# Kernel tuning notes

Hardware: AMD Instinct MI355X
Metric: run time of the kernel (lower is better)

The kernel has to match this reference:

```python
import jax, jax.numpy as jnp
import numpy as np

N, D_IN, D_OUT = 4096, 1024, 1024


def setup_inputs() -> dict:
    key = jax.random.key(0)
    kx, kq, kk, kv = jax.random.split(key, 4)
    s = 1.0 / np.sqrt(D_IN)
    return {
        "x": jax.random.normal(kx, (N, D_IN), dtype=jnp.float32),
        "Wq": jax.random.normal(kq, (D_OUT, D_IN), dtype=jnp.float32) * s,
        "Wk": jax.random.normal(kk, (D_OUT, D_IN), dtype=jnp.float32) * s,
        "Wv": jax.random.normal(kv, (D_OUT, D_IN), dtype=jnp.float32) * s,
    }


def reference(x, Wq, Wk, Wv):
    # nn.Linear(d_in, d_out, bias=False): y = x @ W.T with W: [d_out, d_in]
    q = x @ Wq.T            # [N, d_out]
    k = x @ Wk.T            # [N, d_out]
    v = x @ Wv.T            # [N, d_out]
    scores = q @ k.T        # [N, N]
    scale = 1.0 / jnp.sqrt(jnp.asarray(k.shape[-1], dtype=x.dtype))
    attn = jax.nn.softmax(scores * scale, axis=-1)
    return attn @ v         # [N, d_out]
```

## Files before the change

### kernel.cpp

```cpp
#include <hip/hip_runtime.h>


typedef __attribute__((ext_vector_type(8))) __bf16 bf16x8;
typedef __attribute__((ext_vector_type(4))) float floatx4;

#define GLB_AS __attribute__((address_space(1)))
#define LDS_AS __attribute__((address_space(3)))

static __device__ __forceinline__ unsigned short f2bf_u16(float f) {
  union { float f; unsigned u; } x; x.f = f;
  unsigned r = x.u;
  r += 0x7fffu + ((r >> 16) & 1u);
  return (unsigned short)(r >> 16);
}
static __device__ __forceinline__ float bf2f(unsigned short u) {
  union { unsigned u; float f; } x; x.u = ((unsigned)u) << 16; return x.f;
}

__global__ __launch_bounds__(256) void zero_rs(float* __restrict__ rs) {
  ((float4*)rs)[blockIdx.x * 256 + threadIdx.x] = make_float4(0.f, 0.f, 0.f, 0.f);
}

__global__ __launch_bounds__(256) void cast_all(const float* __restrict__ x,
                                                const float* __restrict__ Wq,
                                                const float* __restrict__ Wk,
                                                const float* __restrict__ Wv,
                                                unsigned short* __restrict__ xb,
                                                unsigned short* __restrict__ wb) {
  const int i = blockIdx.x * 256 + threadIdx.x;
  const int NX4 = 4096 * 1024 / 4;
  const int NW4 = 1024 * 1024 / 4;
  const float* src; unsigned short* dst; int k;
  if (i < NX4)                { src = x;  dst = xb; k = i; }
  else if (i < NX4 + NW4)     { src = Wq; dst = wb;                 k = i - NX4; }
  else if (i < NX4 + 2 * NW4) { src = Wk; dst = wb + 1024 * 1024;   k = i - NX4 - NW4; }
  else                        { src = Wv; dst = wb + 2 * 1024 * 1024; k = i - NX4 - 2 * NW4; }
  float4 v = reinterpret_cast<const float4*>(src)[k];
  ushort4 o = make_ushort4(f2bf_u16(v.x), f2bf_u16(v.y), f2bf_u16(v.z), f2bf_u16(v.w));
  reinterpret_cast<ushort4*>(dst)[k] = o;
}

struct GemmOuts { void* c[4]; int ldc[4]; };

template <int EPI>
__global__ __launch_bounds__(512, 2) void gemm256(const unsigned short* __restrict__ A,
                                                  const unsigned short* __restrict__ B,
                                                  GemmOuts outs, int lda, int ldb,
                                                  int klen, float scale) {
  __shared__ unsigned short sh[65536];
  const int t = threadIdx.x;
  const int w = t >> 6, lane = t & 63;
  const int wm = w >> 2, wn = w & 3;
  const int gx = gridDim.x;
  const int nwg = gx * gridDim.y;
  int bid = blockIdx.y * gx + blockIdx.x;
  bid = (bid & 7) * (nwg >> 3) + (bid >> 3);
  const int row0 = (bid / gx) * 256;
  const int col0 = (bid % gx) * 256;
  const int z = blockIdx.z;
  const int kstart = z * klen;
  const int NT = klen >> 6;

  const int scbe = (((t & 3) ^ ((t >> 3) & 3)) << 3);
  const unsigned short* gA0 = A + (size_t)(row0 + (t >> 2)) * lda + kstart + scbe;
  const unsigned short* gA1 = gA0 + (size_t)128 * lda;
  const unsigned short* gB0 = B + (size_t)(col0 + (t >> 2)) * ldb + kstart + scbe;
  const unsigned short* gB1 = gB0 + (size_t)128 * ldb;

#define STAGE_HALF(h_) do { \
    const int tile_ = (h_) >> 2, opb_ = (h_) & 1, kh_ = ((h_) >> 1) & 1; \
    const int lo_ = (((tile_) & 1) << 15) + (opb_ << 14) + (kh_ << 13) + (w << 9); \
    const unsigned short* s0_ = (opb_ ? gB0 : gA0) + tile_ * 64 + kh_ * 32; \
    const unsigned short* s1_ = (opb_ ? gB1 : gA1) + tile_ * 64 + kh_ * 32; \
    __builtin_amdgcn_global_load_lds((const GLB_AS void*)s0_, (LDS_AS void*)&sh[lo_], 16, 0, 0); \
    __builtin_amdgcn_global_load_lds((const GLB_AS void*)s1_, (LDS_AS void*)&sh[lo_ + 4096], 16, 0, 0); \
  } while (0)
#define STAGE_IF(h_) do { const int hh_ = (h_); if (hh_ < 4 * NT) STAGE_HALF(hh_); } while (0)

  const int fr = lane & 15;
  const int sg = (((lane >> 4) ^ ((lane >> 1) & 3)) << 3);
  int aofs[8], bofs[4];
#pragma unroll
  for (int mf = 0; mf < 8; ++mf) aofs[mf] = ((wm * 128 + mf * 16 + fr) << 5) + sg;
#pragma unroll
  for (int nf = 0; nf < 4; ++nf) bofs[nf] = 16384 + ((wn * 64 + nf * 16 + fr) << 5) + sg;

  floatx4 acc[8][4] = {};

#pragma unroll
  for (int h = 0; h < 7; ++h) STAGE_IF(h);
  asm volatile("s_waitcnt vmcnt(6)" ::: "memory");
  __builtin_amdgcn_s_barrier();

  for (int tile = 0; tile < NT; ++tile) {
    const int bo = (tile & 1) << 15;
    bf16x8 a0[8], b0[2], b1[2];

#pragma unroll
    for (int mf = 0; mf < 8; ++mf) a0[mf] = *(const bf16x8*)&sh[bo + aofs[mf]];
    b0[0] = *(const bf16x8*)&sh[bo + bofs[0]];
    b0[1] = *(const bf16x8*)&sh[bo + bofs[1]];
    STAGE_IF(4 * tile + 7);
    __builtin_amdgcn_s_barrier();
    asm volatile("s_waitcnt lgkmcnt(0)" ::: "memory");
    __builtin_amdgcn_sched_barrier(0);
    __builtin_amdgcn_s_setprio(1);
#pragma unroll
    for (int mf = 0; mf < 8; ++mf)
#pragma unroll
      for (int nf = 0; nf < 2; ++nf)
        acc[mf][nf] = __builtin_amdgcn_mfma_f32_16x16x32_bf16(a0[mf], b0[nf], acc[mf][nf], 0, 0, 0);
    __builtin_amdgcn_s_setprio(0);
    __builtin_amdgcn_s_barrier();

    b1[0] = *(const bf16x8*)&sh[bo + bofs[2]];
    b1[1] = *(const bf16x8*)&sh[bo + bofs[3]];
    STAGE_IF(4 * tile + 8);
    __builtin_amdgcn_s_barrier();
    asm volatile("s_waitcnt lgkmcnt(0)" ::: "memory");
    __builtin_amdgcn_sched_barrier(0);
    __builtin_amdgcn_s_setprio(1);
#pragma unroll
    for (int mf = 0; mf < 8; ++mf)
#pragma unroll
      for (int nf = 0; nf < 2; ++nf)
        acc[mf][2 + nf] = __builtin_amdgcn_mfma_f32_16x16x32_bf16(a0[mf], b1[nf], acc[mf][2 + nf], 0, 0, 0);
    __builtin_amdgcn_s_setprio(0);
    __builtin_amdgcn_s_barrier();

#pragma unroll
    for (int mf = 0; mf < 8; ++mf) a0[mf] = *(const bf16x8*)&sh[bo + 8192 + aofs[mf]];
    b0[0] = *(const bf16x8*)&sh[bo + 8192 + bofs[0]];
    b0[1] = *(const bf16x8*)&sh[bo + 8192 + bofs[1]];
    STAGE_IF(4 * tile + 9);
    __builtin_amdgcn_s_barrier();
    asm volatile("s_waitcnt lgkmcnt(0)" ::: "memory");
    __builtin_amdgcn_sched_barrier(0);
    __builtin_amdgcn_s_setprio(1);
#pragma unroll
    for (int mf = 0; mf < 8; ++mf)
#pragma unroll
      for (int nf = 0; nf < 2; ++nf)
        acc[mf][nf] = __builtin_amdgcn_mfma_f32_16x16x32_bf16(a0[mf], b0[nf], acc[mf][nf], 0, 0, 0);
    __builtin_amdgcn_s_setprio(0);
    __builtin_amdgcn_s_barrier();

    b1[0] = *(const bf16x8*)&sh[bo + 8192 + bofs[2]];
    b1[1] = *(const bf16x8*)&sh[bo + 8192 + bofs[3]];
    STAGE_IF(4 * tile + 10);
    __builtin_amdgcn_s_barrier();
    asm volatile("s_waitcnt lgkmcnt(0)" ::: "memory");
    __builtin_amdgcn_sched_barrier(0);
    __builtin_amdgcn_s_setprio(1);
#pragma unroll
    for (int mf = 0; mf < 8; ++mf)
#pragma unroll
      for (int nf = 0; nf < 2; ++nf)
        acc[mf][2 + nf] = __builtin_amdgcn_mfma_f32_16x16x32_bf16(a0[mf], b1[nf], acc[mf][2 + nf], 0, 0, 0);
    __builtin_amdgcn_s_setprio(0);
    if (tile < NT - 2)       { asm volatile("s_waitcnt vmcnt(6)" ::: "memory"); }
    else if (tile == NT - 2) { asm volatile("s_waitcnt vmcnt(0)" ::: "memory"); }
    __builtin_amdgcn_s_barrier();
  }

#undef STAGE_HALF
#undef STAGE_IF

  const int er = (lane >> 4) * 4;
  const int ec = lane & 15;

  if (EPI == 0) {
    if (z == 0) {
      float* Cf = (float*)outs.c[0];
      const int ldc = outs.ldc[0];
#pragma unroll
      for (int mf = 0; mf < 8; ++mf)
#pragma unroll
        for (int nf = 0; nf < 4; ++nf)
#pragma unroll
          for (int r = 0; r < 4; ++r)
            Cf[(size_t)(row0 + wm * 128 + mf * 16 + er + r) * ldc +
               (col0 + wn * 64 + nf * 16 + ec)] = acc[mf][nf][r] * scale;
    } else {
      unsigned short* Cb = (unsigned short*)outs.c[z];
      const int ldc = outs.ldc[z];
#pragma unroll
      for (int mf = 0; mf < 8; ++mf)
#pragma unroll
        for (int nf = 0; nf < 4; ++nf)
#pragma unroll
          for (int r = 0; r < 4; ++r)
            Cb[(size_t)(row0 + wm * 128 + mf * 16 + er + r) * ldc +
               (col0 + wn * 64 + nf * 16 + ec)] = f2bf_u16(acc[mf][nf][r] * scale);
    }
  } else if (EPI == 2) {
    unsigned short* Pb = (unsigned short*)outs.c[0];
    float* rsp = (float*)outs.c[1];
    const int ldc = outs.ldc[0];
#pragma unroll
    for (int mf = 0; mf < 8; ++mf) {
#pragma unroll
      for (int r = 0; r < 4; ++r) {
        const int m = row0 + wm * 128 + mf * 16 + er + r;
        float rsum = 0.f;
#pragma unroll
        for (int nf = 0; nf < 4; ++nf) {
          const float e = __expf(acc[mf][nf][r] * scale);
          Pb[(size_t)m * ldc + (col0 + wn * 64 + nf * 16 + ec)] = f2bf_u16(e);
          rsum += e;
        }
        rsum += __shfl_xor(rsum, 1);
        rsum += __shfl_xor(rsum, 2);
        rsum += __shfl_xor(rsum, 4);
        rsum += __shfl_xor(rsum, 8);
        if (ec == 0) atomicAdd(rsp + m, rsum);
      }
    }
  } else {
    if (col0 < 2048) {
      unsigned short* qkb = (unsigned short*)outs.c[0];
#pragma unroll
      for (int mf = 0; mf < 8; ++mf)
#pragma unroll
        for (int nf = 0; nf < 4; ++nf)
#pragma unroll
          for (int r = 0; r < 4; ++r)
            qkb[(size_t)(row0 + wm * 128 + mf * 16 + er + r) * 2048 +
                (col0 + wn * 64 + nf * 16 + ec)] = f2bf_u16(acc[mf][nf][r] * scale);
    } else {
      unsigned short* vT = (unsigned short*)outs.c[1];
#pragma unroll
      for (int mf = 0; mf < 8; ++mf)
#pragma unroll
        for (int nf = 0; nf < 4; ++nf) {
          const int n = (col0 - 2048) + wn * 64 + nf * 16 + ec;
          const int mb = row0 + wm * 128 + mf * 16 + er;
          ushort4 o = make_ushort4(f2bf_u16(acc[mf][nf][0] * scale),
                                   f2bf_u16(acc[mf][nf][1] * scale),
                                   f2bf_u16(acc[mf][nf][2] * scale),
                                   f2bf_u16(acc[mf][nf][3] * scale));
          *reinterpret_cast<ushort4*>(&vT[(size_t)n * 4096 + mb]) = o;
        }
    }
  }
}

__global__ __launch_bounds__(256) void reduce_pv(float* __restrict__ out,
                                                 const unsigned short* __restrict__ p1,
                                                 const unsigned short* __restrict__ p2,
                                                 const unsigned short* __restrict__ p3,
                                                 const float* __restrict__ rs) {
  const int row = blockIdx.x;
  const int idx = row * 256 + threadIdx.x;
  const float inv = 1.0f / rs[row];
  float4 o = ((const float4*)out)[idx];
  ushort4 a = ((const ushort4*)p1)[idx];
  ushort4 b = ((const ushort4*)p2)[idx];
  ushort4 c = ((const ushort4*)p3)[idx];
  o.x = (o.x + bf2f(a.x) + bf2f(b.x) + bf2f(c.x)) * inv;
  o.y = (o.y + bf2f(a.y) + bf2f(b.y) + bf2f(c.y)) * inv;
  o.z = (o.z + bf2f(a.z) + bf2f(b.z) + bf2f(c.z)) * inv;
  o.w = (o.w + bf2f(a.w) + bf2f(b.w) + bf2f(c.w)) * inv;
  ((float4*)out)[idx] = o;
}

extern "C" void kernel_launch(void* const* d_in, const int* in_sizes, int n_in,
                              void* d_out, int out_size, void* d_ws, size_t ws_size,
                              hipStream_t stream) {
  const float* x  = (const float*)d_in[0];
  const float* Wq = (const float*)d_in[1];
  const float* Wk = (const float*)d_in[2];
  const float* Wv = (const float*)d_in[3];
  float* out = (float*)d_out;

  const int N = 4096, D = 1024;

  char* ws = (char*)d_ws;
  unsigned short* P   = (unsigned short*)ws;
  unsigned short* qkb = (unsigned short*)(ws + (32u << 20));
  unsigned short* vT  = (unsigned short*)(ws + (48u << 20));
  unsigned short* xb  = (unsigned short*)(ws + (56u << 20));
  unsigned short* wb  = (unsigned short*)(ws + (64u << 20));
  float*          rs  = (float*)(ws + (70u << 20));
  unsigned short* p1  = (unsigned short*)(ws + (72u << 20));
  unsigned short* p2  = (unsigned short*)(ws + (80u << 20));
  unsigned short* p3  = (unsigned short*)(ws + (88u << 20));

  zero_rs<<<4, 256, 0, stream>>>(rs);

  cast_all<<<7168, 256, 0, stream>>>(x, Wq, Wk, Wv, xb, wb);

  GemmOuts oq; oq.c[0] = qkb; oq.c[1] = vT; oq.c[2] = oq.c[3] = qkb;
  oq.ldc[0] = 2048; oq.ldc[1] = 4096; oq.ldc[2] = oq.ldc[3] = 2048;
  gemm256<3><<<dim3(3 * D / 256, N / 256, 1), 512, 0, stream>>>(xb, wb, oq, D, D, D, 1.0f);

  GemmOuts os; os.c[0] = P; os.c[1] = rs; os.c[2] = os.c[3] = P;
  os.ldc[0] = N; os.ldc[1] = 0; os.ldc[2] = os.ldc[3] = N;
  gemm256<2><<<dim3(N / 256, N / 256, 1), 512, 0, stream>>>(qkb, qkb + D, os, 2 * D, 2 * D, D, 0.03125f);

  GemmOuts op;
  op.c[0] = out; op.ldc[0] = D;
  op.c[1] = p1;  op.ldc[1] = D;
  op.c[2] = p2;  op.ldc[2] = D;
  op.c[3] = p3;  op.ldc[3] = D;
  gemm256<0><<<dim3(D / 256, N / 256, 4), 512, 0, stream>>>(P, vT, op, N, N, N / 4, 1.0f);

  reduce_pv<<<N, 256, 0, stream>>>(out, p1, p2, p3, rs);
}
```

Measured before the change: 150.4 us.

## Shrink GEMM tiles to 128x128 and replace atomic row-sum with partial buffer

Replaces the 256x256, 512-thread GEMM with a 128x128, 256-thread kernel that uses a simple double-buffered K=32 pipeline and a smaller LDS footprint, so more blocks fit per CU. Softmax row sums are written as per-column-block partials and reduced in reduce_pv, which removes the zero_rs launch and the atomics. All four split-K PV partials are now bf16, with the first reusing the xb buffer. The smaller tiles add global and LDS traffic per FLOP and drop the fine-grained setprio/sched_barrier interleaving, and storing the first partial in bf16 lowers precision.

```diff
diff --git a/kernel.cpp b/kernel.cpp
--- a/kernel.cpp
+++ b/kernel.cpp
@@ -15,10 +15,6 @@
 }
 static __device__ __forceinline__ float bf2f(unsigned short u) {
   union { unsigned u; float f; } x; x.u = ((unsigned)u) << 16; return x.f;
-}
-
-__global__ __launch_bounds__(256) void zero_rs(float* __restrict__ rs) {
-  ((float4*)rs)[blockIdx.x * 256 + threadIdx.x] = make_float4(0.f, 0.f, 0.f, 0.f);
 }
 
 __global__ __launch_bounds__(256) void cast_all(const float* __restrict__ x,
@@ -31,9 +27,9 @@
   const int NX4 = 4096 * 1024 / 4;
   const int NW4 = 1024 * 1024 / 4;
   const float* src; unsigned short* dst; int k;
-  if (i < NX4)                { src = x;  dst = xb; k = i; }
-  else if (i < NX4 + NW4)     { src = Wq; dst = wb;                 k = i - NX4; }
-  else if (i < NX4 + 2 * NW4) { src = Wk; dst = wb + 1024 * 1024;   k = i - NX4 - NW4; }
+  if (i < NX4)                { src = x;  dst = xb;                   k = i; }
+  else if (i < NX4 + NW4)     { src = Wq; dst = wb;                   k = i - NX4; }
+  else if (i < NX4 + 2 * NW4) { src = Wk; dst = wb + 1024 * 1024;     k = i - NX4 - NW4; }
   else                        { src = Wv; dst = wb + 2 * 1024 * 1024; k = i - NX4 - 2 * NW4; }
   float4 v = reinterpret_cast<const float4*>(src)[k];
   ushort4 o = make_ushort4(f2bf_u16(v.x), f2bf_u16(v.y), f2bf_u16(v.z), f2bf_u16(v.w));
@@ -43,165 +39,104 @@
 struct GemmOuts { void* c[4]; int ldc[4]; };
 
 template <int EPI>
-__global__ __launch_bounds__(512, 2) void gemm256(const unsigned short* __restrict__ A,
+__global__ __launch_bounds__(256, 4) void gemm128(const unsigned short* __restrict__ A,
                                                   const unsigned short* __restrict__ B,
                                                   GemmOuts outs, int lda, int ldb,
                                                   int klen, float scale) {
-  __shared__ unsigned short sh[65536];
+  __shared__ unsigned short sh[16384];
   const int t = threadIdx.x;
   const int w = t >> 6, lane = t & 63;
-  const int wm = w >> 2, wn = w & 3;
+  const int wm = w >> 1, wn = w & 1;
   const int gx = gridDim.x;
   const int nwg = gx * gridDim.y;
   int bid = blockIdx.y * gx + blockIdx.x;
   bid = (bid & 7) * (nwg >> 3) + (bid >> 3);
-  const int row0 = (bid / gx) * 256;
-  const int col0 = (bid % gx) * 256;
+  const int row0 = (bid / gx) * 128;
+  const int col0 = (bid % gx) * 128;
   const int z = blockIdx.z;
   const int kstart = z * klen;
-  const int NT = klen >> 6;
-
+  const int NT = klen >> 5;
+
+  const int srow = t >> 2;
   const int scbe = (((t & 3) ^ ((t >> 3) & 3)) << 3);
-  const unsigned short* gA0 = A + (size_t)(row0 + (t >> 2)) * lda + kstart + scbe;
-  const unsigned short* gA1 = gA0 + (size_t)128 * lda;
-  const unsigned short* gB0 = B + (size_t)(col0 + (t >> 2)) * ldb + kstart + scbe;
-  const unsigned short* gB1 = gB0 + (size_t)128 * ldb;
-
-#define STAGE_HALF(h_) do { \
-    const int tile_ = (h_) >> 2, opb_ = (h_) & 1, kh_ = ((h_) >> 1) & 1; \
-    const int lo_ = (((tile_) & 1) << 15) + (opb_ << 14) + (kh_ << 13) + (w << 9); \
-    const unsigned short* s0_ = (opb_ ? gB0 : gA0) + tile_ * 64 + kh_ * 32; \
-    const unsigned short* s1_ = (opb_ ? gB1 : gA1) + tile_ * 64 + kh_ * 32; \
-    __builtin_amdgcn_global_load_lds((const GLB_AS void*)s0_, (LDS_AS void*)&sh[lo_], 16, 0, 0); \
-    __builtin_amdgcn_global_load_lds((const GLB_AS void*)s1_, (LDS_AS void*)&sh[lo_ + 4096], 16, 0, 0); \
+  const unsigned short* gA0 = A + (size_t)(row0 + srow) * lda + kstart + scbe;
+  const unsigned short* gA1 = gA0 + (size_t)64 * lda;
+  const unsigned short* gB0 = B + (size_t)(col0 + srow) * ldb + kstart + scbe;
+  const unsigned short* gB1 = gB0 + (size_t)64 * ldb;
+
+#define STAGE(tl_) do { \
+    const int bb_ = ((tl_) & 1) * 8192; \
+    __builtin_amdgcn_global_load_lds((const GLB_AS void*)(gA0 + (tl_) * 32), \
+        (LDS_AS void*)&sh[bb_ + t * 8], 16, 0, 0); \
+    __builtin_amdgcn_global_load_lds((const GLB_AS void*)(gA1 + (tl_) * 32), \
+        (LDS_AS void*)&sh[bb_ + 2048 + t * 8], 16, 0, 0); \
+    __builtin_amdgcn_global_load_lds((const GLB_AS void*)(gB0 + (tl_) * 32), \
+        (LDS_AS void*)&sh[bb_ + 4096 + t * 8], 16, 0, 0); \
+    __builtin_amdgcn_global_load_lds((const GLB_AS void*)(gB1 + (tl_) * 32), \
+        (LDS_AS void*)&sh[bb_ + 6144 + t * 8], 16, 0, 0); \
   } while (0)
-#define STAGE_IF(h_) do { const int hh_ = (h_); if (hh_ < 4 * NT) STAGE_HALF(hh_); } while (0)
 
   const int fr = lane & 15;
   const int sg = (((lane >> 4) ^ ((lane >> 1) & 3)) << 3);
-  int aofs[8], bofs[4];
-#pragma unroll
-  for (int mf = 0; mf < 8; ++mf) aofs[mf] = ((wm * 128 + mf * 16 + fr) << 5) + sg;
-#pragma unroll
-  for (int nf = 0; nf < 4; ++nf) bofs[nf] = 16384 + ((wn * 64 + nf * 16 + fr) << 5) + sg;
-
-  floatx4 acc[8][4] = {};
-
-#pragma unroll
-  for (int h = 0; h < 7; ++h) STAGE_IF(h);
-  asm volatile("s_waitcnt vmcnt(6)" ::: "memory");
-  __builtin_amdgcn_s_barrier();
+  int aofs[4], bofs[4];
+#pragma unroll
+  for (int mf = 0; mf < 4; ++mf) aofs[mf] = ((wm * 64 + mf * 16 + fr) << 5) + sg;
+#pragma unroll
+  for (int nf = 0; nf < 4; ++nf) bofs[nf] = 4096 + ((wn * 64 + nf * 16 + fr) << 5) + sg;
+
+  floatx4 acc[4][4] = {};
+
+  STAGE(0);
 
   for (int tile = 0; tile < NT; ++tile) {
-    const int bo = (tile & 1) << 15;
-    bf16x8 a0[8], b0[2], b1[2];
-
-#pragma unroll
-    for (int mf = 0; mf < 8; ++mf) a0[mf] = *(const bf16x8*)&sh[bo + aofs[mf]];
-    b0[0] = *(const bf16x8*)&sh[bo + bofs[0]];
-    b0[1] = *(const bf16x8*)&sh[bo + bofs[1]];
-    STAGE_IF(4 * tile + 7);
+    if (tile + 1 < NT) {
+      STAGE(tile + 1);
+      asm volatile("s_waitcnt vmcnt(4)" ::: "memory");
+    } else {
+      asm volatile("s_waitcnt vmcnt(0)" ::: "memory");
+    }
     __builtin_amdgcn_s_barrier();
-    asm volatile("s_waitcnt lgkmcnt(0)" ::: "memory");
-    __builtin_amdgcn_sched_barrier(0);
-    __builtin_amdgcn_s_setprio(1);
-#pragma unroll
-    for (int mf = 0; mf < 8; ++mf)
-#pragma unroll
-      for (int nf = 0; nf < 2; ++nf)
-        acc[mf][nf] = __builtin_amdgcn_mfma_f32_16x16x32_bf16(a0[mf], b0[nf], acc[mf][nf], 0, 0, 0);
-    __builtin_amdgcn_s_setprio(0);
-    __builtin_amdgcn_s_barrier();
-
-    b1[0] = *(const bf16x8*)&sh[bo + bofs[2]];
-    b1[1] = *(const bf16x8*)&sh[bo + bofs[3]];
-    STAGE_IF(4 * tile + 8);
-    __builtin_amdgcn_s_barrier();
-    asm volatile("s_waitcnt lgkmcnt(0)" ::: "memory");
-    __builtin_amdgcn_sched_barrier(0);
-    __builtin_amdgcn_s_setprio(1);
-#pragma unroll
-    for (int mf = 0; mf < 8; ++mf)
-#pragma unroll
-      for (int nf = 0; nf < 2; ++nf)
-        acc[mf][2 + nf] = __builtin_amdgcn_mfma_f32_16x16x32_bf16(a0[mf], b1[nf], acc[mf][2 + nf], 0, 0, 0);
-    __builtin_amdgcn_s_setprio(0);
-    __builtin_amdgcn_s_barrier();
-
-#pragma unroll
-    for (int mf = 0; mf < 8; ++mf) a0[mf] = *(const bf16x8*)&sh[bo + 8192 + aofs[mf]];
-    b0[0] = *(const bf16x8*)&sh[bo + 8192 + bofs[0]];
-    b0[1] = *(const bf16x8*)&sh[bo + 8192 + bofs[1]];
-    STAGE_IF(4 * tile + 9);
-    __builtin_amdgcn_s_barrier();
-    asm volatile("s_waitcnt lgkmcnt(0)" ::: "memory");
-    __builtin_amdgcn_sched_barrier(0);
-    __builtin_amdgcn_s_setprio(1);
-#pragma unroll
-    for (int mf = 0; mf < 8; ++mf)
-#pragma unroll
-      for (int nf = 0; nf < 2; ++nf)
-        acc[mf][nf] = __builtin_amdgcn_mfma_f32_16x16x32_bf16(a0[mf], b0[nf], acc[mf][nf], 0, 0, 0);
-    __builtin_amdgcn_s_setprio(0);
-    __builtin_amdgcn_s_barrier();
-
-    b1[0] = *(const bf16x8*)&sh[bo + 8192 + bofs[2]];
-    b1[1] = *(const bf16x8*)&sh[bo + 8192 + bofs[3]];
-    STAGE_IF(4 * tile + 10);
-    __builtin_amdgcn_s_barrier();
-    asm volatile("s_waitcnt lgkmcnt(0)" ::: "memory");
-    __builtin_amdgcn_sched_barrier(0);
-    __builtin_amdgcn_s_setprio(1);
-#pragma unroll
-    for (int mf = 0; mf < 8; ++mf)
-#pragma unroll
-      for (int nf = 0; nf < 2; ++nf)
-        acc[mf][2 + nf] = __builtin_amdgcn_mfma_f32_16x16x32_bf16(a0[mf], b1[nf], acc[mf][2 + nf], 0, 0, 0);
-    __builtin_amdgcn_s_setprio(0);
-    if (tile < NT - 2)       { asm volatile("s_waitcnt vmcnt(6)" ::: "memory"); }
-    else if (tile == NT - 2) { asm volatile("s_waitcnt vmcnt(0)" ::: "memory"); }
+
+    const int bo = (tile & 1) * 8192;
+    bf16x8 af[4], bf[4];
+#pragma unroll
+    for (int mf = 0; mf < 4; ++mf) af[mf] = *(const bf16x8*)&sh[bo + aofs[mf]];
+#pragma unroll
+    for (int nf = 0; nf < 4; ++nf) bf[nf] = *(const bf16x8*)&sh[bo + bofs[nf]];
+#pragma unroll
+    for (int mf = 0; mf < 4; ++mf)
+#pragma unroll
+      for (int nf = 0; nf < 4; ++nf)
+        acc[mf][nf] = __builtin_amdgcn_mfma_f32_16x16x32_bf16(af[mf], bf[nf], acc[mf][nf], 0, 0, 0);
+
     __builtin_amdgcn_s_barrier();
   }
-
-#undef STAGE_HALF
-#undef STAGE_IF
+#undef STAGE
 
   const int er = (lane >> 4) * 4;
   const int ec = lane & 15;
 
   if (EPI == 0) {
-    if (z == 0) {
-      float* Cf = (float*)outs.c[0];
-      const int ldc = outs.ldc[0];
-#pragma unroll
-      for (int mf = 0; mf < 8; ++mf)
-#pragma unroll
-        for (int nf = 0; nf < 4; ++nf)
-#pragma unroll
-          for (int r = 0; r < 4; ++r)
-            Cf[(size_t)(row0 + wm * 128 + mf * 16 + er + r) * ldc +
-               (col0 + wn * 64 + nf * 16 + ec)] = acc[mf][nf][r] * scale;
-    } else {
-      unsigned short* Cb = (unsigned short*)outs.c[z];
-      const int ldc = outs.ldc[z];
-#pragma unroll
-      for (int mf = 0; mf < 8; ++mf)
-#pragma unroll
-        for (int nf = 0; nf < 4; ++nf)
-#pragma unroll
-          for (int r = 0; r < 4; ++r)
-            Cb[(size_t)(row0 + wm * 128 + mf * 16 + er + r) * ldc +
-               (col0 + wn * 64 + nf * 16 + ec)] = f2bf_u16(acc[mf][nf][r] * scale);
-    }
+    unsigned short* Cb = (unsigned short*)outs.c[z];
+    const int ldc = outs.ldc[z];
+#pragma unroll
+    for (int mf = 0; mf < 4; ++mf)
+#pragma unroll
+      for (int nf = 0; nf < 4; ++nf)
+#pragma unroll
+        for (int r = 0; r < 4; ++r)
+          Cb[(size_t)(row0 + wm * 64 + mf * 16 + er + r) * ldc +
+             (col0 + wn * 64 + nf * 16 + ec)] = f2bf_u16(acc[mf][nf][r] * scale);
   } else if (EPI == 2) {
     unsigned short* Pb = (unsigned short*)outs.c[0];
     float* rsp = (float*)outs.c[1];
     const int ldc = outs.ldc[0];
-#pragma unroll
-    for (int mf = 0; mf < 8; ++mf) {
+    const int rj = ((col0 >> 7) * 2 + wn) * 4096;
+#pragma unroll
+    for (int mf = 0; mf < 4; ++mf) {
 #pragma unroll
       for (int r = 0; r < 4; ++r) {
-        const int m = row0 + wm * 128 + mf * 16 + er + r;
+        const int m = row0 + wm * 64 + mf * 16 + er + r;
         float rsum = 0.f;
 #pragma unroll
         for (int nf = 0; nf < 4; ++nf) {
@@ -213,28 +148,28 @@
         rsum += __shfl_xor(rsum, 2);
         rsum += __shfl_xor(rsum, 4);
         rsum += __shfl_xor(rsum, 8);
-        if (ec == 0) atomicAdd(rsp + m, rsum);
+        if (ec == 0) rsp[rj + m] = rsum;
       }
     }
   } else {
     if (col0 < 2048) {
       unsigned short* qkb = (unsigned short*)outs.c[0];
 #pragma unroll
-      for (int mf = 0; mf < 8; ++mf)
+      for (int mf = 0; mf < 4; ++mf)
 #pragma unroll
         for (int nf = 0; nf < 4; ++nf)
 #pragma unroll
           for (int r = 0; r < 4; ++r)
-            qkb[(size_t)(row0 + wm * 128 + mf * 16 + er + r) * 2048 +
+            qkb[(size_t)(row0 + wm * 64 + mf * 16 + er + r) * 2048 +
                 (col0 + wn * 64 + nf * 16 + ec)] = f2bf_u16(acc[mf][nf][r] * scale);
     } else {
       unsigned short* vT = (unsigned short*)outs.c[1];
 #pragma unroll
-      for (int mf = 0; mf < 8; ++mf)
+      for (int mf = 0; mf < 4; ++mf)
 #pragma unroll
         for (int nf = 0; nf < 4; ++nf) {
           const int n = (col0 - 2048) + wn * 64 + nf * 16 + ec;
-          const int mb = row0 + wm * 128 + mf * 16 + er;
+          const int mb = row0 + wm * 64 + mf * 16 + er;
           ushort4 o = make_ushort4(f2bf_u16(acc[mf][nf][0] * scale),
                                    f2bf_u16(acc[mf][nf][1] * scale),
                                    f2bf_u16(acc[mf][nf][2] * scale),
@@ -246,21 +181,27 @@
 }
 
 __global__ __launch_bounds__(256) void reduce_pv(float* __restrict__ out,
+                                                 const unsigned short* __restrict__ p0,
                                                  const unsigned short* __restrict__ p1,
                                                  const unsigned short* __restrict__ p2,
                                                  const unsigned short* __restrict__ p3,
-                                                 const float* __restrict__ rs) {
+                                                 const float* __restrict__ rsp) {
   const int row = blockIdx.x;
+  const int lane = threadIdx.x & 63;
+  float s = rsp[lane * 4096 + row];
+#pragma unroll
+  for (int off = 32; off >= 1; off >>= 1) s += __shfl_xor(s, off);
+  const float inv = 1.0f / s;
   const int idx = row * 256 + threadIdx.x;
-  const float inv = 1.0f / rs[row];
-  float4 o = ((const float4*)out)[idx];
-  ushort4 a = ((const ushort4*)p1)[idx];
-  ushort4 b = ((const ushort4*)p2)[idx];
-  ushort4 c = ((const ushort4*)p3)[idx];
-  o.x = (o.x + bf2f(a.x) + bf2f(b.x) + bf2f(c.x)) * inv;
-  o.y = (o.y + bf2f(a.y) + bf2f(b.y) + bf2f(c.y)) * inv;
-  o.z = (o.z + bf2f(a.z) + bf2f(b.z) + bf2f(c.z)) * inv;
-  o.w = (o.w + bf2f(a.w) + bf2f(b.w) + bf2f(c.w)) * inv;
+  ushort4 a = ((const ushort4*)p0)[idx];
+  ushort4 b = ((const ushort4*)p1)[idx];
+  ushort4 c = ((const ushort4*)p2)[idx];
+  ushort4 d = ((const ushort4*)p3)[idx];
+  float4 o;
+  o.x = (bf2f(a.x) + bf2f(b.x) + bf2f(c.x) + bf2f(d.x)) * inv;
+  o.y = (bf2f(a.y) + bf2f(b.y) + bf2f(c.y) + bf2f(d.y)) * inv;
+  o.z = (bf2f(a.z) + bf2f(b.z) + bf2f(c.z) + bf2f(d.z)) * inv;
+  o.w = (bf2f(a.w) + bf2f(b.w) + bf2f(c.w) + bf2f(d.w)) * inv;
   ((float4*)out)[idx] = o;
 }
 
@@ -281,29 +222,28 @@
   unsigned short* vT  = (unsigned short*)(ws + (48u << 20));
   unsigned short* xb  = (unsigned short*)(ws + (56u << 20));
   unsigned short* wb  = (unsigned short*)(ws + (64u << 20));
-  float*          rs  = (float*)(ws + (70u << 20));
+  float*          rsp = (float*)(ws + (70u << 20));
+  unsigned short* p0  = xb;
   unsigned short* p1  = (unsigned short*)(ws + (72u << 20));
   unsigned short* p2  = (unsigned short*)(ws + (80u << 20));
   unsigned short* p3  = (unsigned short*)(ws + (88u << 20));
 
-  zero_rs<<<4, 256, 0, stream>>>(rs);
-
   cast_all<<<7168, 256, 0, stream>>>(x, Wq, Wk, Wv, xb, wb);
 
   GemmOuts oq; oq.c[0] = qkb; oq.c[1] = vT; oq.c[2] = oq.c[3] = qkb;
   oq.ldc[0] = 2048; oq.ldc[1] = 4096; oq.ldc[2] = oq.ldc[3] = 2048;
-  gemm256<3><<<dim3(3 * D / 256, N / 256, 1), 512, 0, stream>>>(xb, wb, oq, D, D, D, 1.0f);
-
-  GemmOuts os; os.c[0] = P; os.c[1] = rs; os.c[2] = os.c[3] = P;
+  gemm128<3><<<dim3(3 * D / 128, N / 128, 1), 256, 0, stream>>>(xb, wb, oq, D, D, D, 1.0f);
+
+  GemmOuts os; os.c[0] = P; os.c[1] = rsp; os.c[2] = os.c[3] = P;
   os.ldc[0] = N; os.ldc[1] = 0; os.ldc[2] = os.ldc[3] = N;
-  gemm256<2><<<dim3(N / 256, N / 256, 1), 512, 0, stream>>>(qkb, qkb + D, os, 2 * D, 2 * D, D, 0.03125f);
+  gemm128<2><<<dim3(N / 128, N / 128, 1), 256, 0, stream>>>(qkb, qkb + D, os, 2 * D, 2 * D, D, 0.03125f);
 
   GemmOuts op;
-  op.c[0] = out; op.ldc[0] = D;
-  op.c[1] = p1;  op.ldc[1] = D;
-  op.c[2] = p2;  op.ldc[2] = D;
-  op.c[3] = p3;  op.ldc[3] = D;
-  gemm256<0><<<dim3(D / 256, N / 256, 4), 512, 0, stream>>>(P, vT, op, N, N, N / 4, 1.0f);
-
-  reduce_pv<<<N, 256, 0, stream>>>(out, p1, p2, p3, rs);
-}
+  op.c[0] = p0; op.ldc[0] = D;
+  op.c[1] = p1; op.ldc[1] = D;
+  op.c[2] = p2; op.ldc[2] = D;
+  op.c[3] = p3; op.ldc[3] = D;
+  gemm128<0><<<dim3(D / 128, N / 128, 4), 256, 0, stream>>>(P, vT, op, N, N, N / 4, 1.0f);
+
+  reduce_pv<<<N, 256, 0, stream>>>(out, p0, p1, p2, p3, rsp);
+}
```

Measured after the change: 153.1 us. About the same (+1.8%).
